# Kernel tuning notes

Hardware: AMD Instinct MI355X
Metric: run time of the kernel (lower is better)

Reference implementation:

```python
import jax, jax.numpy as jnp
import numpy as np

IDIM, NCH, ODIM = 512, 256, 3
B, W = 64, 1024


def _gru_cell(x, h, w_ih, w_hh, b_ih, b_hh):
    # PyTorch GRU gate order: r, z, n
    gi = x @ w_ih.T + b_ih
    gh = h @ w_hh.T + b_hh
    i_r, i_z, i_n = jnp.split(gi, 3, axis=-1)
    h_r, h_z, h_n = jnp.split(gh, 3, axis=-1)
    r = jax.nn.sigmoid(i_r + h_r)
    z = jax.nn.sigmoid(i_z + h_z)
    n = jnp.tanh(i_n + r * h_n)
    return (1.0 - z) * n + z * h


def setup_inputs() -> dict:
    key = jax.random.key(0)
    ks = jax.random.split(key, 14)
    s = 0.05
    return {
        "x": jax.random.normal(ks[0], (B, W, IDIM), dtype=jnp.float32),
        "embed_w": jax.random.normal(ks[1], (NCH, ODIM), dtype=jnp.float32) * s,
        "embed_b": jnp.zeros((NCH,), dtype=jnp.float32),
        "w_ih0": jax.random.normal(ks[2], (3 * NCH, IDIM + NCH), dtype=jnp.float32) * s,
        "w_hh0": jax.random.normal(ks[3], (3 * NCH, NCH), dtype=jnp.float32) * s,
        "b_ih0": jnp.zeros((3 * NCH,), dtype=jnp.float32),
        "b_hh0": jnp.zeros((3 * NCH,), dtype=jnp.float32),
        "w_ih1": jax.random.normal(ks[4], (3 * NCH, NCH), dtype=jnp.float32) * s,
        "w_hh1": jax.random.normal(ks[5], (3 * NCH, NCH), dtype=jnp.float32) * s,
        "b_ih1": jnp.zeros((3 * NCH,), dtype=jnp.float32),
        "b_hh1": jnp.zeros((3 * NCH,), dtype=jnp.float32),
        "proj_w": jax.random.normal(ks[6], (ODIM, NCH), dtype=jnp.float32) * s,
        "proj_b": jnp.zeros((ODIM,), dtype=jnp.float32),
    }


def reference(x, embed_w, embed_b, w_ih0, w_hh0, b_ih0, b_hh0,
              w_ih1, w_hh1, b_ih1, b_hh1, proj_w, proj_b):
    # at each step t, embed previous sigmoid VAD output, concat with x_t,
    # run 2-layer GRU single step, project + sigmoid.
    b = x.shape[0]
    h0_init = jnp.zeros((b, NCH), dtype=x.dtype)
    h1_init = jnp.zeros((b, NCH), dtype=x.dtype)
    v_init = jnp.zeros((b, ODIM), dtype=x.dtype)

    def step(carry, x_t):
        h0, h1, prev_v = carry
        emb = prev_v @ embed_w.T + embed_b                 # [B, NCH]
        inp = jnp.concatenate([x_t, emb], axis=-1)         # [B, IDIM+NCH]
        h0 = _gru_cell(inp, h0, w_ih0, w_hh0, b_ih0, b_hh0)
        h1 = _gru_cell(h0, h1, w_ih1, w_hh1, b_ih1, b_hh1)
        v = jax.nn.sigmoid(h1 @ proj_w.T + proj_b)         # [B, ODIM]
        return (h0, h1, v), v

    xs = jnp.transpose(x, (1, 0, 2))  # [W, B, IDIM]
    _, ys = jax.lax.scan(step, (h0_init, h1_init, v_init), xs)
    return jnp.transpose(ys, (1, 0, 2))  # [B, W, ODIM]
```

## Files before the change

kernel.cpp:

```cpp
#include <hip/hip_runtime.h>

#define T_FULL 1024
#define NBATCH 64
#define IDIM   512
#define NCH    256
#define GD     768
#define ODIM   3
#define NBLK   16

typedef _Float16 half8   __attribute__((ext_vector_type(8)));
typedef float    floatx4 __attribute__((ext_vector_type(4)));

__device__ __forceinline__ float sigmoidf_(float x) { return 1.0f / (1.0f + __expf(-x)); }
__device__ __forceinline__ float tanhf_(float x)    { return 1.0f - 2.0f / (__expf(2.0f * x) + 1.0f); }

__device__ __forceinline__ floatx4 splat4(float v) { floatx4 r; r[0]=v; r[1]=v; r[2]=v; r[3]=v; return r; }

__device__ __forceinline__ half8 cvt8(const float* __restrict__ p) {
  floatx4 a = *(const floatx4*)p;
  floatx4 b = *(const floatx4*)(p + 4);
  half8 h;
  h[0]=(_Float16)a[0]; h[1]=(_Float16)a[1]; h[2]=(_Float16)a[2]; h[3]=(_Float16)a[3];
  h[4]=(_Float16)b[0]; h[5]=(_Float16)b[1]; h[6]=(_Float16)b[2]; h[7]=(_Float16)b[3];
  return h;
}

__global__ __launch_bounds__(256)
void xw_gemm(const float* __restrict__ x, const float* __restrict__ w_ih0,
             _Float16* __restrict__ Xw, int t0, int Tc) {
  __shared__ _Float16 As[128 * 32];
  __shared__ _Float16 Bs[128 * 32];
  const int tid  = threadIdx.x;
  const int lane = tid & 63;
  const int wave = tid >> 6;
  const int lq = lane >> 4, lc = lane & 15;
  const int wm = wave >> 1, wn = wave & 1;

  const int sr = tid >> 1;
  const int sh = (tid & 1) * 16;
  const int m  = blockIdx.x * 128 + sr;
  const float* arow = x + ((size_t)(m & 63) * T_FULL + (size_t)(t0 + (m >> 6))) * IDIM;
  const float* brow = w_ih0 + (size_t)(blockIdx.y * 128 + sr) * GD;

  floatx4 acc[4][4];
  #pragma unroll
  for (int i = 0; i < 4; ++i)
    #pragma unroll
    for (int j = 0; j < 4; ++j) acc[i][j] = splat4(0.f);

  for (int kk = 0; kk < IDIM; kk += 32) {
    __syncthreads();
    #pragma unroll
    for (int kb = 0; kb < 2; ++kb) {
      const int k0  = sh + kb * 8;
      const int gis = (k0 >> 3) ^ ((sr >> 2) & 3);
      *(half8*)((char*)As + sr * 64 + gis * 16) = cvt8(arow + kk + k0);
      *(half8*)((char*)Bs + sr * 64 + gis * 16) = cvt8(brow + kk + k0);
    }
    __syncthreads();
    half8 af[4], bf[4];
    #pragma unroll
    for (int ms = 0; ms < 4; ++ms) {
      const int r = wm * 64 + ms * 16 + lc;
      af[ms] = *(const half8*)((char*)As + r * 64 + ((lq ^ ((r >> 2) & 3)) * 16));
    }
    #pragma unroll
    for (int ns = 0; ns < 4; ++ns) {
      const int r = wn * 64 + ns * 16 + lc;
      bf[ns] = *(const half8*)((char*)Bs + r * 64 + ((lq ^ ((r >> 2) & 3)) * 16));
    }
    #pragma unroll
    for (int ms = 0; ms < 4; ++ms)
      #pragma unroll
      for (int ns = 0; ns < 4; ++ns)
        acc[ms][ns] = __builtin_amdgcn_mfma_f32_16x16x32_f16(af[ms], bf[ns], acc[ms][ns], 0, 0, 0);
  }

  #pragma unroll
  for (int ms = 0; ms < 4; ++ms)
    #pragma unroll
    for (int ns = 0; ns < 4; ++ns)
      #pragma unroll
      for (int q = 0; q < 4; ++q) {
        const int mloc = blockIdx.x * 128 + wm * 64 + ms * 16 + lq * 4 + q;
        const int g    = blockIdx.y * 128 + wn * 64 + ns * 16 + lc;
        Xw[(size_t)mloc * GD + g] = (_Float16)acc[ms][ns][q];
      }
}

__device__ __forceinline__ void grid_barrier(unsigned int* flags, int blk, unsigned int ep) {
  __syncthreads();
  if (threadIdx.x == 0) {
    __builtin_amdgcn_fence(__ATOMIC_RELEASE, "agent");
    __hip_atomic_store(&flags[blk * 32], ep, __ATOMIC_RELAXED, __HIP_MEMORY_SCOPE_AGENT);
  }
  if (threadIdx.x < 64) {
    const int lane = threadIdx.x;
    const int idx  = (lane < NBLK) ? lane * 32 : 0;
    int spins = 0;
    for (;;) {
      unsigned int v = __hip_atomic_load(&flags[idx], __ATOMIC_RELAXED, __HIP_MEMORY_SCOPE_AGENT);
      if (lane >= NBLK) v = ep;
      if (__all((int)(v >= ep))) break;
      if (++spins > (1 << 16)) break;
      __builtin_amdgcn_s_sleep(1);
    }
    __builtin_amdgcn_fence(__ATOMIC_ACQUIRE, "agent");
  }
  __syncthreads();
}

__global__ __launch_bounds__(256, 1)
void rec_step(const float* __restrict__ w_ih0, const float* __restrict__ w_hh0,
              const float* __restrict__ w_ih1, const float* __restrict__ w_hh1,
              const float* __restrict__ b_ih0, const float* __restrict__ b_hh0,
              const float* __restrict__ b_ih1, const float* __restrict__ b_hh1,
              const float* __restrict__ embed_w, const float* __restrict__ embed_b,
              const float* __restrict__ proj_w, const float* __restrict__ proj_b,
              const _Float16* __restrict__ Xw, float* __restrict__ out,
              _Float16* h0_pub, _Float16* h1_pub, unsigned int* flags,
              int t0, int Tc, int lastChunk) {
  const int tid  = threadIdx.x;
  const int wave = tid >> 6;
  const int lane = tid & 63;
  const int lq = lane >> 4, lc = lane & 15;
  const int blk = blockIdx.x;
  const int c   = blk * 16 + lc;

  half8 Whh0[3][8], Whh1[3][8], Wih1[3][8], Pj[8];
  #pragma unroll
  for (int g = 0; g < 3; ++g) {
    const int row = g * NCH + c;
    #pragma unroll
    for (int ks = 0; ks < 8; ++ks) {
      const int k0 = ks * 32 + lq * 8;
      Whh0[g][ks] = cvt8(w_hh0 + (size_t)row * NCH + k0);
      Whh1[g][ks] = cvt8(w_hh1 + (size_t)row * NCH + k0);
      Wih1[g][ks] = cvt8(w_ih1 + (size_t)row * NCH + k0);
    }
  }
  #pragma unroll
  for (int ks = 0; ks < 8; ++ks) {
    const int k0 = ks * 32 + lq * 8;
    half8 z;
    #pragma unroll
    for (int j = 0; j < 8; ++j) z[j] = (_Float16)0.f;
    Pj[ks] = (lc < 3) ? cvt8(proj_w + lc * NCH + k0) : z;
  }

  float Wce[3][3], bi0[3], bh0v[3], bi1v[3], bh1v[3];
  #pragma unroll
  for (int g = 0; g < 3; ++g) {
    const int row = g * NCH + c;
    float a0 = 0.f, a1 = 0.f, a2 = 0.f, ab = b_ih0[row];
    const float* wr = w_ih0 + (size_t)row * GD + IDIM;
    for (int k = 0; k < NCH; ++k) {
      const float w = wr[k];
      a0 += w * embed_w[k * 3 + 0];
      a1 += w * embed_w[k * 3 + 1];
      a2 += w * embed_w[k * 3 + 2];
      ab += w * embed_b[k];
    }
    Wce[g][0] = a0; Wce[g][1] = a1; Wce[g][2] = a2;
    bi0[g] = ab;
    bh0v[g] = b_hh0[row]; bi1v[g] = b_ih1[row]; bh1v[g] = b_hh1[row];
  }
  const float pb = (lc < 3) ? proj_b[lc] : 0.f;

  float h0st[4] = {0.f, 0.f, 0.f, 0.f};
  float h1st[4] = {0.f, 0.f, 0.f, 0.f};
  if (t0 > 0) {
    const int rp0 = ((t0 & 1) ^ 1) * (NBATCH * NCH);
    #pragma unroll
    for (int q = 0; q < 4; ++q) {
      const int b = wave * 16 + lq * 4 + q;
      h0st[q] = (float)h0_pub[rp0 + b * NCH + c];
      h1st[q] = (float)h1_pub[rp0 + b * NCH + c];
    }
  }
  floatx4 ag1[3];
  const int arow = (wave * 16 + lc) * NCH;

  for (int lt = 0; lt < Tc; ++lt) {
    const int gt = t0 + lt;
    const int rp = ((gt & 1) ^ 1) * (NBATCH * NCH);
    const int wp = (gt & 1) * (NBATCH * NCH);
    const _Float16* h0r = h0_pub + rp;
    const _Float16* h1r = h1_pub + rp;

    floatx4 ah0[3];
    #pragma unroll
    for (int g = 0; g < 3; ++g) ah0[g] = splat4(bh0v[g]);
    #pragma unroll
    for (int hh = 0; hh < 2; ++hh) {
      half8 ha[4];
      #pragma unroll
      for (int i = 0; i < 4; ++i) ha[i] = *(const half8*)(h0r + arow + (hh * 4 + i) * 32 + lq * 8);
      #pragma unroll
      for (int g = 0; g < 3; ++g)
        #pragma unroll
        for (int i = 0; i < 4; ++i)
          ah0[g] = __builtin_amdgcn_mfma_f32_16x16x32_f16(ha[i], Whh0[g][hh * 4 + i], ah0[g], 0, 0, 0);
    }
    #pragma unroll
    for (int g = 0; g < 3; ++g) ag1[g] = splat4(bh1v[g]);
    floatx4 av = splat4(pb);
    #pragma unroll
    for (int hh = 0; hh < 2; ++hh) {
      half8 ha[4];
      #pragma unroll
      for (int i = 0; i < 4; ++i) ha[i] = *(const half8*)(h1r + arow + (hh * 4 + i) * 32 + lq * 8);
      #pragma unroll
      for (int g = 0; g < 3; ++g)
        #pragma unroll
        for (int i = 0; i < 4; ++i)
          ag1[g] = __builtin_amdgcn_mfma_f32_16x16x32_f16(ha[i], Whh1[g][hh * 4 + i], ag1[g], 0, 0, 0);
      #pragma unroll
      for (int i = 0; i < 4; ++i)
        av = __builtin_amdgcn_mfma_f32_16x16x32_f16(ha[i], Pj[hh * 4 + i], av, 0, 0, 0);
    }
    float vv0[4], vv1[4], vv2[4];
    if (gt == 0) {
      #pragma unroll
      for (int q = 0; q < 4; ++q) { vv0[q] = 0.f; vv1[q] = 0.f; vv2[q] = 0.f; }
    } else {
      float sv[4];
      #pragma unroll
      for (int q = 0; q < 4; ++q) sv[q] = (lc < 3) ? sigmoidf_(av[q]) : 0.f;
      if (blk == 0 && lc < 3) {
        #pragma unroll
        for (int q = 0; q < 4; ++q)
          out[((size_t)(wave * 16 + lq * 4 + q) * T_FULL + (gt - 1)) * ODIM + lc] = sv[q];
      }
      #pragma unroll
      for (int q = 0; q < 4; ++q) {
        vv0[q] = __shfl(sv[q], (lq << 4) + 0, 64);
        vv1[q] = __shfl(sv[q], (lq << 4) + 1, 64);
        vv2[q] = __shfl(sv[q], (lq << 4) + 2, 64);
      }
    }
    const _Float16* xwp = Xw + (size_t)lt * (NBATCH * GD);
    float h0n[4];
    #pragma unroll
    for (int q = 0; q < 4; ++q) {
      const int b = wave * 16 + lq * 4 + q;
      const float i_r = (float)xwp[b * GD + 0 * NCH + c] + bi0[0] + vv0[q] * Wce[0][0] + vv1[q] * Wce[0][1] + vv2[q] * Wce[0][2];
      const float i_z = (float)xwp[b * GD + 1 * NCH + c] + bi0[1] + vv0[q] * Wce[1][0] + vv1[q] * Wce[1][1] + vv2[q] * Wce[1][2];
      const float i_n = (float)xwp[b * GD + 2 * NCH + c] + bi0[2] + vv0[q] * Wce[2][0] + vv1[q] * Wce[2][1] + vv2[q] * Wce[2][2];
      const float r = sigmoidf_(i_r + ah0[0][q]);
      const float z = sigmoidf_(i_z + ah0[1][q]);
      const float n = tanhf_(i_n + r * ah0[2][q]);
      h0n[q] = (1.f - z) * n + z * h0st[q];
      h0st[q] = h0n[q];
    }
    {
      _Float16* h0w = h0_pub + wp;
      #pragma unroll
      for (int q = 0; q < 4; ++q)
        h0w[(wave * 16 + lq * 4 + q) * NCH + c] = (_Float16)h0n[q];
    }
    grid_barrier(flags, blk, (unsigned)(2 * gt + 1));

    const _Float16* h0r2 = h0_pub + wp;
    floatx4 ai1[3];
    #pragma unroll
    for (int g = 0; g < 3; ++g) ai1[g] = splat4(bi1v[g]);
    #pragma unroll
    for (int hh = 0; hh < 2; ++hh) {
      half8 ha[4];
      #pragma unroll
      for (int i = 0; i < 4; ++i) ha[i] = *(const half8*)(h0r2 + arow + (hh * 4 + i) * 32 + lq * 8);
      #pragma unroll
      for (int g = 0; g < 3; ++g)
        #pragma unroll
        for (int i = 0; i < 4; ++i)
          ai1[g] = __builtin_amdgcn_mfma_f32_16x16x32_f16(ha[i], Wih1[g][hh * 4 + i], ai1[g], 0, 0, 0);
    }
    float h1n[4];
    #pragma unroll
    for (int q = 0; q < 4; ++q) {
      const float r = sigmoidf_(ai1[0][q] + ag1[0][q]);
      const float z = sigmoidf_(ai1[1][q] + ag1[1][q]);
      const float n = tanhf_(ai1[2][q] + r * ag1[2][q]);
      h1n[q] = (1.f - z) * n + z * h1st[q];
      h1st[q] = h1n[q];
    }
    {
      _Float16* h1w = h1_pub + wp;
      #pragma unroll
      for (int q = 0; q < 4; ++q)
        h1w[(wave * 16 + lq * 4 + q) * NCH + c] = (_Float16)h1n[q];
    }
    grid_barrier(flags, blk, (unsigned)(2 * gt + 2));
  }

  if (lastChunk && blk == 0) {
    const _Float16* h1r = h1_pub + (((t0 + Tc - 1) & 1)) * (NBATCH * NCH);
    floatx4 av = splat4(pb);
    #pragma unroll
    for (int ks = 0; ks < 8; ++ks) {
      half8 ha = *(const half8*)(h1r + arow + ks * 32 + lq * 8);
      av = __builtin_amdgcn_mfma_f32_16x16x32_f16(ha, Pj[ks], av, 0, 0, 0);
    }
    if (lc < 3) {
      #pragma unroll
      for (int q = 0; q < 4; ++q)
        out[((size_t)(wave * 16 + lq * 4 + q) * T_FULL + (T_FULL - 1)) * ODIM + lc] = sigmoidf_(av[q]);
    }
  }
}

extern "C" void kernel_launch(void* const* d_in, const int* in_sizes, int n_in,
                              void* d_out, int out_size, void* d_ws, size_t ws_size,
                              hipStream_t stream) {
  const float* x       = (const float*)d_in[0];
  const float* embed_w = (const float*)d_in[1];
  const float* embed_b = (const float*)d_in[2];
  const float* w_ih0   = (const float*)d_in[3];
  const float* w_hh0   = (const float*)d_in[4];
  const float* b_ih0   = (const float*)d_in[5];
  const float* b_hh0   = (const float*)d_in[6];
  const float* w_ih1   = (const float*)d_in[7];
  const float* w_hh1   = (const float*)d_in[8];
  const float* b_ih1   = (const float*)d_in[9];
  const float* b_hh1   = (const float*)d_in[10];
  const float* proj_w  = (const float*)d_in[11];
  const float* proj_b  = (const float*)d_in[12];
  float* out = (float*)d_out;

  char* ws = (char*)d_ws;
  _Float16* h0_pub = (_Float16*)(ws);
  _Float16* h1_pub = (_Float16*)(ws + 65536);
  unsigned int* flags = (unsigned int*)(ws + 131072);
  _Float16* Xw = (_Float16*)(ws + 262144);

  const size_t per_t = (size_t)NBATCH * GD * sizeof(_Float16);
  size_t xw_avail = (ws_size > 262144) ? (ws_size - 262144) : 0;
  long maxTc = (long)(xw_avail / per_t);
  int Tc = 2;
  while ((long)Tc * 2 <= maxTc && Tc * 2 <= T_FULL) Tc *= 2;

  hipMemsetAsync(ws, 0, 262144, stream);

  for (int t0 = 0; t0 < T_FULL; t0 += Tc) {
    dim3 g1(Tc * NBATCH / 128, GD / 128);
    xw_gemm<<<g1, 256, 0, stream>>>(x, w_ih0, Xw, t0, Tc);
    rec_step<<<NBLK, 256, 0, stream>>>(w_ih0, w_hh0, w_ih1, w_hh1,
                                       b_ih0, b_hh0, b_ih1, b_hh1,
                                       embed_w, embed_b, proj_w, proj_b,
                                       Xw, out, h0_pub, h1_pub, flags,
                                       t0, Tc, (t0 + Tc) >= T_FULL ? 1 : 0);
  }
}
```

Before: 10.19 ms.

## Replace grid barriers with tagged hidden-state publish and per-wave polling

Removes the flag-based grid barrier. Each hidden-state value is now published as a 64-bit word holding the fp16 data pair plus a timestep tag. Consumers poll directly on the data with cache-bypassing loads until all tags match, so sync and data transfer are fused and each wave waits only for what it needs. The Xw layout is rearranged so each block reads a contiguous per-block tile, and the h1 work is reordered ahead of h0. This doubles the bytes moved for state and adds spin-polling traffic, and the bounded spin can silently read stale data on timeout.

```diff
diff --git a/kernel.cpp b/kernel.cpp
--- a/kernel.cpp
+++ b/kernel.cpp
@@ -10,10 +10,11 @@
 
 typedef _Float16 half8   __attribute__((ext_vector_type(8)));
 typedef float    floatx4 __attribute__((ext_vector_type(4)));
+typedef unsigned int uintx4 __attribute__((ext_vector_type(4)));
+typedef unsigned int uintx2 __attribute__((ext_vector_type(2)));
 
 __device__ __forceinline__ float sigmoidf_(float x) { return 1.0f / (1.0f + __expf(-x)); }
 __device__ __forceinline__ float tanhf_(float x)    { return 1.0f - 2.0f / (__expf(2.0f * x) + 1.0f); }
-
 __device__ __forceinline__ floatx4 splat4(float v) { floatx4 r; r[0]=v; r[1]=v; r[2]=v; r[3]=v; return r; }
 
 __device__ __forceinline__ half8 cvt8(const float* __restrict__ p) {
@@ -83,31 +84,65 @@
       #pragma unroll
       for (int q = 0; q < 4; ++q) {
         const int mloc = blockIdx.x * 128 + wm * 64 + ms * 16 + lq * 4 + q;
-        const int g    = blockIdx.y * 128 + wn * 64 + ns * 16 + lc;
-        Xw[(size_t)mloc * GD + g] = (_Float16)acc[ms][ns][q];
+        const int gp   = blockIdx.y * 128 + wn * 64 + ns * 16 + lc;
+        const int t = mloc >> 6, b = mloc & 63;
+        const int gate = gp >> 8, cch = gp & 255;
+        Xw[(((size_t)t * NBLK + (cch >> 4)) * 3 + gate) * 1024 + b * 16 + (cch & 15)]
+            = (_Float16)acc[ms][ns][q];
       }
 }
 
-__device__ __forceinline__ void grid_barrier(unsigned int* flags, int blk, unsigned int ep) {
-  __syncthreads();
-  if (threadIdx.x == 0) {
-    __builtin_amdgcn_fence(__ATOMIC_RELEASE, "agent");
-    __hip_atomic_store(&flags[blk * 32], ep, __ATOMIC_RELAXED, __HIP_MEMORY_SCOPE_AGENT);
-  }
-  if (threadIdx.x < 64) {
-    const int lane = threadIdx.x;
-    const int idx  = (lane < NBLK) ? lane * 32 : 0;
-    int spins = 0;
-    for (;;) {
-      unsigned int v = __hip_atomic_load(&flags[idx], __ATOMIC_RELAXED, __HIP_MEMORY_SCOPE_AGENT);
-      if (lane >= NBLK) v = ep;
-      if (__all((int)(v >= ep))) break;
-      if (++spins > (1 << 16)) break;
-      __builtin_amdgcn_s_sleep(1);
-    }
-    __builtin_amdgcn_fence(__ATOMIC_ACQUIRE, "agent");
-  }
-  __syncthreads();
+__device__ __forceinline__ void poll_group(const char* __restrict__ pb, int boff,
+                                           unsigned exp, half8* __restrict__ out) {
+  uintx4 A[16];
+  int cap = 1 << 18;
+  for (;;) {
+    #pragma unroll
+    for (int f = 0; f < 8; ++f) {
+      const char* p0 = pb + boff + f * 128;
+      asm volatile("global_load_dwordx4 %0, %1, off sc0 sc1"
+                   : "=v"(A[2 * f]) : "v"(p0) : "memory");
+      asm volatile("global_load_dwordx4 %0, %1, off sc0 sc1"
+                   : "=v"(A[2 * f + 1]) : "v"(p0 + 16) : "memory");
+    }
+    asm volatile("s_waitcnt vmcnt(0)" ::: "memory");
+    __builtin_amdgcn_sched_barrier(0);
+    bool ok = true;
+    #pragma unroll
+    for (int j = 0; j < 16; ++j) ok = ok && (A[j].y == exp) && (A[j].w == exp);
+    if (__all((int)ok) || --cap <= 0) break;
+  }
+  #pragma unroll
+  for (int f = 0; f < 8; ++f) {
+    uintx4 t;
+    t.x = A[2 * f].x;     t.y = A[2 * f].z;
+    t.z = A[2 * f + 1].x; t.w = A[2 * f + 1].z;
+    out[f] = __builtin_bit_cast(half8, t);
+  }
+}
+
+__device__ __forceinline__ void publish4(char* __restrict__ base, int wave, int lq, int lc,
+                                         int blk, unsigned tag, const float* __restrict__ hv) {
+  float pv[4];
+  #pragma unroll
+  for (int q = 0; q < 4; ++q) pv[q] = __shfl_xor(hv[q], 1, 64);
+  unsigned dq[4];
+  #pragma unroll
+  for (int q = 0; q < 4; ++q) {
+    _Float16 a = (_Float16)hv[q], p = (_Float16)pv[q];
+    unsigned au = __builtin_bit_cast(unsigned short, a);
+    unsigned pu = __builtin_bit_cast(unsigned short, p);
+    dq[q] = (lc & 1) ? (pu | (au << 16)) : (au | (pu << 16));
+  }
+  const int q0 = (lc & 1) ? 2 : 0;
+  #pragma unroll
+  for (int s = 0; s < 2; ++s) {
+    const int q = q0 + s;
+    char* addr = base + (((wave * 16 + lq * 4 + q) * 128) + blk * 8 + (lc >> 1)) * 8;
+    uintx2 v; v.x = dq[q]; v.y = tag;
+    asm volatile("global_store_dwordx2 %0, %1, off sc0 sc1"
+                 :: "v"(addr), "v"(v) : "memory");
+  }
 }
 
 __global__ __launch_bounds__(256, 1)
@@ -118,7 +153,7 @@
               const float* __restrict__ embed_w, const float* __restrict__ embed_b,
               const float* __restrict__ proj_w, const float* __restrict__ proj_b,
               const _Float16* __restrict__ Xw, float* __restrict__ out,
-              _Float16* h0_pub, _Float16* h1_pub, unsigned int* flags,
+              char* h0b, char* h1b,
               int t0, int Tc, int lastChunk) {
   const int tid  = threadIdx.x;
   const int wave = tid >> 6;
@@ -170,55 +205,61 @@
   float h0st[4] = {0.f, 0.f, 0.f, 0.f};
   float h1st[4] = {0.f, 0.f, 0.f, 0.f};
   if (t0 > 0) {
-    const int rp0 = ((t0 & 1) ^ 1) * (NBATCH * NCH);
+    const int rpo = ((t0 & 1) ^ 1) * 65536;
+    const unsigned long long* p0 = (const unsigned long long*)(h0b + rpo);
+    const unsigned long long* p1 = (const unsigned long long*)(h1b + rpo);
     #pragma unroll
     for (int q = 0; q < 4; ++q) {
-      const int b = wave * 16 + lq * 4 + q;
-      h0st[q] = (float)h0_pub[rp0 + b * NCH + c];
-      h1st[q] = (float)h1_pub[rp0 + b * NCH + c];
-    }
-  }
-  floatx4 ag1[3];
-  const int arow = (wave * 16 + lc) * NCH;
+      const int b   = wave * 16 + lq * 4 + q;
+      const int idx = b * 128 + blk * 8 + (lc >> 1);
+      unsigned d0 = (unsigned)p0[idx], d1 = (unsigned)p1[idx];
+      unsigned short u0 = (lc & 1) ? (unsigned short)(d0 >> 16) : (unsigned short)(d0 & 0xffff);
+      unsigned short u1 = (lc & 1) ? (unsigned short)(d1 >> 16) : (unsigned short)(d1 & 0xffff);
+      h0st[q] = (float)__builtin_bit_cast(_Float16, u0);
+      h1st[q] = (float)__builtin_bit_cast(_Float16, u1);
+    }
+  }
+
+  const int boff = (wave * 16 + lc) * 1024 + lq * 32;
+  floatx4 ag1l[3];
+  half8 hf[8];
 
   for (int lt = 0; lt < Tc; ++lt) {
     const int gt = t0 + lt;
-    const int rp = ((gt & 1) ^ 1) * (NBATCH * NCH);
-    const int wp = (gt & 1) * (NBATCH * NCH);
-    const _Float16* h0r = h0_pub + rp;
-    const _Float16* h1r = h1_pub + rp;
-
+    const int rp = ((gt & 1) ^ 1) * 65536;
+    const int wp = (gt & 1) * 65536;
+    const unsigned expt = (unsigned)gt;
+
+    const _Float16* xb = Xw + ((size_t)lt * NBLK + blk) * 3072;
+    unsigned short xwu[3][4];
+    #pragma unroll
+    for (int g = 0; g < 3; ++g)
+      #pragma unroll
+      for (int q = 0; q < 4; ++q)
+        xwu[g][q] = *(const unsigned short*)(xb + g * 1024 + (wave * 16 + lq * 4 + q) * 16 + lc);
+
+    poll_group(h1b + rp, boff, expt, hf);
+    floatx4 av = splat4(pb);
+    #pragma unroll
+    for (int g = 0; g < 3; ++g) ag1l[g] = splat4(bh1v[g]);
+    #pragma unroll
+    for (int ks = 0; ks < 8; ++ks) {
+      #pragma unroll
+      for (int g = 0; g < 3; ++g)
+        ag1l[g] = __builtin_amdgcn_mfma_f32_16x16x32_f16(hf[ks], Whh1[g][ks], ag1l[g], 0, 0, 0);
+      av = __builtin_amdgcn_mfma_f32_16x16x32_f16(hf[ks], Pj[ks], av, 0, 0, 0);
+    }
+
+    poll_group(h0b + rp, boff, expt, hf);
     floatx4 ah0[3];
     #pragma unroll
     for (int g = 0; g < 3; ++g) ah0[g] = splat4(bh0v[g]);
     #pragma unroll
-    for (int hh = 0; hh < 2; ++hh) {
-      half8 ha[4];
-      #pragma unroll
-      for (int i = 0; i < 4; ++i) ha[i] = *(const half8*)(h0r + arow + (hh * 4 + i) * 32 + lq * 8);
+    for (int ks = 0; ks < 8; ++ks)
       #pragma unroll
       for (int g = 0; g < 3; ++g)
-        #pragma unroll
-        for (int i = 0; i < 4; ++i)
-          ah0[g] = __builtin_amdgcn_mfma_f32_16x16x32_f16(ha[i], Whh0[g][hh * 4 + i], ah0[g], 0, 0, 0);
-    }
-    #pragma unroll
-    for (int g = 0; g < 3; ++g) ag1[g] = splat4(bh1v[g]);
-    floatx4 av = splat4(pb);
-    #pragma unroll
-    for (int hh = 0; hh < 2; ++hh) {
-      half8 ha[4];
-      #pragma unroll
-      for (int i = 0; i < 4; ++i) ha[i] = *(const half8*)(h1r + arow + (hh * 4 + i) * 32 + lq * 8);
-      #pragma unroll
-      for (int g = 0; g < 3; ++g)
-        #pragma unroll
-        for (int i = 0; i < 4; ++i)
-          ag1[g] = __builtin_amdgcn_mfma_f32_16x16x32_f16(ha[i], Whh1[g][hh * 4 + i], ag1[g], 0, 0, 0);
-      #pragma unroll
-      for (int i = 0; i < 4; ++i)
-        av = __builtin_amdgcn_mfma_f32_16x16x32_f16(ha[i], Pj[hh * 4 + i], av, 0, 0, 0);
-    }
+        ah0[g] = __builtin_amdgcn_mfma_f32_16x16x32_f16(hf[ks], Whh0[g][ks], ah0[g], 0, 0, 0);
+
     float vv0[4], vv1[4], vv2[4];
     if (gt == 0) {
       #pragma unroll
@@ -239,73 +280,57 @@
         vv2[q] = __shfl(sv[q], (lq << 4) + 2, 64);
       }
     }
-    const _Float16* xwp = Xw + (size_t)lt * (NBATCH * GD);
+
     float h0n[4];
     #pragma unroll
     for (int q = 0; q < 4; ++q) {
-      const int b = wave * 16 + lq * 4 + q;
-      const float i_r = (float)xwp[b * GD + 0 * NCH + c] + bi0[0] + vv0[q] * Wce[0][0] + vv1[q] * Wce[0][1] + vv2[q] * Wce[0][2];
-      const float i_z = (float)xwp[b * GD + 1 * NCH + c] + bi0[1] + vv0[q] * Wce[1][0] + vv1[q] * Wce[1][1] + vv2[q] * Wce[1][2];
-      const float i_n = (float)xwp[b * GD + 2 * NCH + c] + bi0[2] + vv0[q] * Wce[2][0] + vv1[q] * Wce[2][1] + vv2[q] * Wce[2][2];
+      const float i_r = (float)__builtin_bit_cast(_Float16, xwu[0][q]) + bi0[0]
+                        + vv0[q] * Wce[0][0] + vv1[q] * Wce[0][1] + vv2[q] * Wce[0][2];
+      const float i_z = (float)__builtin_bit_cast(_Float16, xwu[1][q]) + bi0[1]
+                        + vv0[q] * Wce[1][0] + vv1[q] * Wce[1][1] + vv2[q] * Wce[1][2];
+      const float i_n = (float)__builtin_bit_cast(_Float16, xwu[2][q]) + bi0[2]
+                        + vv0[q] * Wce[2][0] + vv1[q] * Wce[2][1] + vv2[q] * Wce[2][2];
       const float r = sigmoidf_(i_r + ah0[0][q]);
       const float z = sigmoidf_(i_z + ah0[1][q]);
       const float n = tanhf_(i_n + r * ah0[2][q]);
       h0n[q] = (1.f - z) * n + z * h0st[q];
       h0st[q] = h0n[q];
     }
-    {
-      _Float16* h0w = h0_pub + wp;
-      #pragma unroll
-      for (int q = 0; q < 4; ++q)
-        h0w[(wave * 16 + lq * 4 + q) * NCH + c] = (_Float16)h0n[q];
-    }
-    grid_barrier(flags, blk, (unsigned)(2 * gt + 1));
-
-    const _Float16* h0r2 = h0_pub + wp;
+    publish4(h0b + wp, wave, lq, lc, blk, (unsigned)(gt + 1), h0n);
+
+    poll_group(h0b + wp, boff, (unsigned)(gt + 1), hf);
     floatx4 ai1[3];
     #pragma unroll
     for (int g = 0; g < 3; ++g) ai1[g] = splat4(bi1v[g]);
     #pragma unroll
-    for (int hh = 0; hh < 2; ++hh) {
-      half8 ha[4];
-      #pragma unroll
-      for (int i = 0; i < 4; ++i) ha[i] = *(const half8*)(h0r2 + arow + (hh * 4 + i) * 32 + lq * 8);
+    for (int ks = 0; ks < 8; ++ks)
       #pragma unroll
       for (int g = 0; g < 3; ++g)
-        #pragma unroll
-        for (int i = 0; i < 4; ++i)
-          ai1[g] = __builtin_amdgcn_mfma_f32_16x16x32_f16(ha[i], Wih1[g][hh * 4 + i], ai1[g], 0, 0, 0);
-    }
+        ai1[g] = __builtin_amdgcn_mfma_f32_16x16x32_f16(hf[ks], Wih1[g][ks], ai1[g], 0, 0, 0);
+
     float h1n[4];
     #pragma unroll
     for (int q = 0; q < 4; ++q) {
-      const float r = sigmoidf_(ai1[0][q] + ag1[0][q]);
-      const float z = sigmoidf_(ai1[1][q] + ag1[1][q]);
-      const float n = tanhf_(ai1[2][q] + r * ag1[2][q]);
+      const float r = sigmoidf_(ai1[0][q] + ag1l[0][q]);
+      const float z = sigmoidf_(ai1[1][q] + ag1l[1][q]);
+      const float n = tanhf_(ai1[2][q] + r * ag1l[2][q]);
       h1n[q] = (1.f - z) * n + z * h1st[q];
       h1st[q] = h1n[q];
     }
-    {
-      _Float16* h1w = h1_pub + wp;
+    publish4(h1b + wp, wave, lq, lc, blk, (unsigned)(gt + 1), h1n);
+  }
+
+  if (lastChunk && blk == 0) {
+    poll_group(h1b + (((t0 + Tc - 1) & 1) * 65536), boff, (unsigned)(t0 + Tc), hf);
+    floatx4 av = splat4(pb);
+    #pragma unroll
+    for (int ks = 0; ks < 8; ++ks)
+      av = __builtin_amdgcn_mfma_f32_16x16x32_f16(hf[ks], Pj[ks], av, 0, 0, 0);
+    if (lc < 3) {
       #pragma unroll
       for (int q = 0; q < 4; ++q)
-        h1w[(wave * 16 + lq * 4 + q) * NCH + c] = (_Float16)h1n[q];
-    }
-    grid_barrier(flags, blk, (unsigned)(2 * gt + 2));
-  }
-
-  if (lastChunk && blk == 0) {
-    const _Float16* h1r = h1_pub + (((t0 + Tc - 1) & 1)) * (NBATCH * NCH);
-    floatx4 av = splat4(pb);
-    #pragma unroll
-    for (int ks = 0; ks < 8; ++ks) {
-      half8 ha = *(const half8*)(h1r + arow + ks * 32 + lq * 8);
-      av = __builtin_amdgcn_mfma_f32_16x16x32_f16(ha, Pj[ks], av, 0, 0, 0);
-    }
-    if (lc < 3) {
-      #pragma unroll
-      for (int q = 0; q < 4; ++q)
-        out[((size_t)(wave * 16 + lq * 4 + q) * T_FULL + (T_FULL - 1)) * ODIM + lc] = sigmoidf_(av[q]);
+        out[((size_t)(wave * 16 + lq * 4 + q) * T_FULL + (T_FULL - 1)) * ODIM + lc]
+            = sigmoidf_(av[q]);
     }
   }
 }
@@ -329,9 +354,8 @@
   float* out = (float*)d_out;
 
   char* ws = (char*)d_ws;
-  _Float16* h0_pub = (_Float16*)(ws);
-  _Float16* h1_pub = (_Float16*)(ws + 65536);
-  unsigned int* flags = (unsigned int*)(ws + 131072);
+  char* h0b = ws;
+  char* h1b = ws + 131072;
   _Float16* Xw = (_Float16*)(ws + 262144);
 
   const size_t per_t = (size_t)NBATCH * GD * sizeof(_Float16);
@@ -348,7 +372,7 @@
     rec_step<<<NBLK, 256, 0, stream>>>(w_ih0, w_hh0, w_ih1, w_hh1,
                                        b_ih0, b_hh0, b_ih1, b_hh1,
                                        embed_w, embed_b, proj_w, proj_b,
-                                       Xw, out, h0_pub, h1_pub, flags,
+                                       Xw, out, h0b, h1b,
                                        t0, Tc, (t0 + Tc) >= T_FULL ? 1 : 0);
   }
 }
```

New measurement: 14.12 ms. +38.6%, slower.

## Split recurrence by batch groups with LDS-resident hidden state, drop grid barriers

Applied to the files above, without the earlier changes.

The recurrent kernel is reorganized so each of 4 workgroups (1024 threads) owns 16 batch rows and all 256 channels. Hidden state is exchanged through double-buffered swizzled LDS, and workgroup __syncthreads replace the cross-block atomic grid barriers. Weight conversion to fp16 in MFMA fragment order and the embedding fold are moved into separate prep kernels. The input-projection GEMM now writes in a tiled layout matching the new fragments. The aim is to remove the global-memory flag spins every timestep, but each workgroup now holds all weights in registers with only 4 CUs active, and large register arrays per thread risk spills.

```diff
diff --git a/kernel.cpp b/kernel.cpp
--- a/kernel.cpp
+++ b/kernel.cpp
@@ -6,14 +6,19 @@
 #define NCH    256
 #define GD     768
 #define ODIM   3
-#define NBLK   16
-
-typedef _Float16 half8   __attribute__((ext_vector_type(8)));
+#define NBG    4
+
+typedef _Float16 half8 __attribute__((ext_vector_type(8)));
+typedef _Float16 half4 __attribute__((ext_vector_type(4)));
 typedef float    floatx4 __attribute__((ext_vector_type(4)));
+
+#define PP_OFF   1179648
+#define WCB_OFF  1187840
+#define HS_OFF   1200128
+#define XW_OFF   1376256
 
 __device__ __forceinline__ float sigmoidf_(float x) { return 1.0f / (1.0f + __expf(-x)); }
 __device__ __forceinline__ float tanhf_(float x)    { return 1.0f - 2.0f / (__expf(2.0f * x) + 1.0f); }
-
 __device__ __forceinline__ floatx4 splat4(float v) { floatx4 r; r[0]=v; r[1]=v; r[2]=v; r[3]=v; return r; }
 
 __device__ __forceinline__ half8 cvt8(const float* __restrict__ p) {
@@ -23,6 +28,53 @@
   h[0]=(_Float16)a[0]; h[1]=(_Float16)a[1]; h[2]=(_Float16)a[2]; h[3]=(_Float16)a[3];
   h[4]=(_Float16)b[0]; h[5]=(_Float16)b[1]; h[6]=(_Float16)b[2]; h[7]=(_Float16)b[3];
   return h;
+}
+
+__global__ __launch_bounds__(256)
+void wprep_w(const float* __restrict__ w_hh0, const float* __restrict__ w_ih1,
+             const float* __restrict__ w_hh1, const float* __restrict__ proj_w,
+             _Float16* __restrict__ Wp, _Float16* __restrict__ Pp) {
+  const int idx = blockIdx.x * 256 + threadIdx.x;
+  if (idx < 73728) {
+    const int m = idx / 24576, r = idx % 24576;
+    const int pt = r / 512, r2 = r % 512;
+    const int ks = r2 / 64, lane = r2 % 64;
+    const int lq = lane >> 4, lc = lane & 15;
+    const int c = (pt / 3) * 16 + lc, g = pt % 3;
+    const float* src = (m == 0 ? w_hh0 : (m == 1 ? w_ih1 : w_hh1))
+                       + (size_t)(g * NCH + c) * NCH + ks * 32 + lq * 8;
+    *(half8*)(Wp + (size_t)idx * 8) = cvt8(src);
+  } else if (idx < 74240) {
+    const int j = idx - 73728;
+    const int ks = j >> 6, lane = j & 63;
+    const int lq = lane >> 4, lc = lane & 15;
+    half8 v;
+    if (lc < 3) v = cvt8(proj_w + lc * NCH + ks * 32 + lq * 8);
+    else { for (int k = 0; k < 8; ++k) v[k] = (_Float16)0.f; }
+    *(half8*)(Pp + (size_t)j * 8) = v;
+  }
+}
+
+__global__ __launch_bounds__(256)
+void wprep_c(const float* __restrict__ w_ih0, const float* __restrict__ embed_w,
+             const float* __restrict__ embed_b, const float* __restrict__ b_ih0,
+             float* __restrict__ Wcb) {
+  const int prow = blockIdx.x * 256 + threadIdx.x;
+  if (prow >= 768) return;
+  const int pt = prow >> 4, lcc = prow & 15;
+  const int c = (pt / 3) * 16 + lcc, g = pt % 3;
+  const int srow = g * NCH + c;
+  const float* wr = w_ih0 + (size_t)srow * GD + IDIM;
+  float a0 = 0.f, a1 = 0.f, a2 = 0.f, ab = b_ih0[srow];
+  for (int k = 0; k < NCH; ++k) {
+    const float w = wr[k];
+    a0 += w * embed_w[k * 3 + 0];
+    a1 += w * embed_w[k * 3 + 1];
+    a2 += w * embed_w[k * 3 + 2];
+    ab += w * embed_b[k];
+  }
+  Wcb[prow * 4 + 0] = a0; Wcb[prow * 4 + 1] = a1;
+  Wcb[prow * 4 + 2] = a2; Wcb[prow * 4 + 3] = ab;
 }
 
 __global__ __launch_bounds__(256)
@@ -83,231 +135,195 @@
       #pragma unroll
       for (int q = 0; q < 4; ++q) {
         const int mloc = blockIdx.x * 128 + wm * 64 + ms * 16 + lq * 4 + q;
-        const int g    = blockIdx.y * 128 + wn * 64 + ns * 16 + lc;
-        Xw[(size_t)mloc * GD + g] = (_Float16)acc[ms][ns][q];
+        const int gp   = blockIdx.y * 128 + wn * 64 + ns * 16 + lc;
+        const int t = mloc >> 6, b = mloc & 63;
+        const int g = gp >> 8, c = gp & 255;
+        const int pt = (c >> 4) * 3 + g;
+        Xw[(((size_t)t * NBG + (b >> 4)) * 48 + pt) * 256 + (c & 15) * 16 + (b & 15)]
+            = (_Float16)acc[ms][ns][q];
       }
 }
 
-__device__ __forceinline__ void grid_barrier(unsigned int* flags, int blk, unsigned int ep) {
-  __syncthreads();
-  if (threadIdx.x == 0) {
-    __builtin_amdgcn_fence(__ATOMIC_RELEASE, "agent");
-    __hip_atomic_store(&flags[blk * 32], ep, __ATOMIC_RELAXED, __HIP_MEMORY_SCOPE_AGENT);
-  }
-  if (threadIdx.x < 64) {
-    const int lane = threadIdx.x;
-    const int idx  = (lane < NBLK) ? lane * 32 : 0;
-    int spins = 0;
-    for (;;) {
-      unsigned int v = __hip_atomic_load(&flags[idx], __ATOMIC_RELAXED, __HIP_MEMORY_SCOPE_AGENT);
-      if (lane >= NBLK) v = ep;
-      if (__all((int)(v >= ep))) break;
-      if (++spins > (1 << 16)) break;
-      __builtin_amdgcn_s_sleep(1);
-    }
-    __builtin_amdgcn_fence(__ATOMIC_ACQUIRE, "agent");
-  }
-  __syncthreads();
-}
-
-__global__ __launch_bounds__(256, 1)
-void rec_step(const float* __restrict__ w_ih0, const float* __restrict__ w_hh0,
-              const float* __restrict__ w_ih1, const float* __restrict__ w_hh1,
-              const float* __restrict__ b_ih0, const float* __restrict__ b_hh0,
-              const float* __restrict__ b_ih1, const float* __restrict__ b_hh1,
-              const float* __restrict__ embed_w, const float* __restrict__ embed_b,
-              const float* __restrict__ proj_w, const float* __restrict__ proj_b,
-              const _Float16* __restrict__ Xw, float* __restrict__ out,
-              _Float16* h0_pub, _Float16* h1_pub, unsigned int* flags,
-              int t0, int Tc, int lastChunk) {
+__global__ __launch_bounds__(1024, 4)
+void rec_r(const _Float16* __restrict__ Wp, const _Float16* __restrict__ Pp,
+           const float* __restrict__ Wcb,
+           const float* __restrict__ b_hh0, const float* __restrict__ b_ih1,
+           const float* __restrict__ b_hh1, const float* __restrict__ proj_b,
+           const _Float16* __restrict__ Xw, float* __restrict__ out,
+           float* __restrict__ hs, int t0, int Tc, int lastChunk) {
+  __shared__ __align__(16) _Float16 hl[2][2][4096];
+  __shared__ __align__(16) float v_lds[64];
   const int tid  = threadIdx.x;
   const int wave = tid >> 6;
   const int lane = tid & 63;
   const int lq = lane >> 4, lc = lane & 15;
-  const int blk = blockIdx.x;
-  const int c   = blk * 16 + lc;
-
-  half8 Whh0[3][8], Whh1[3][8], Wih1[3][8], Pj[8];
+  const int bg = blockIdx.x;
+  const int ch = wave * 16 + lc;
+
+  #define HBYTE(b, k) ((b) * 512 + (((k) * 2) ^ (((b) & 7) << 4)))
+  #define LDA(layer, par, ks) \
+    (*(const half8*)((const char*)(&hl[layer][par][0]) + lc * 512 + ((((ks) * 64) + lq * 16) ^ ((lc & 7) << 4))))
+
+  half8 W0[3][8], W1[3][8], W2[3][8], Pj[8];
+  #pragma unroll
+  for (int g = 0; g < 3; ++g)
+    #pragma unroll
+    for (int ks = 0; ks < 8; ++ks) {
+      const size_t base = ((size_t)(wave * 3 + g) * 512 + ks * 64 + lane) * 8;
+      W0[g][ks] = *(const half8*)(Wp + base);
+      W1[g][ks] = *(const half8*)(Wp + 196608 + base);
+      W2[g][ks] = *(const half8*)(Wp + 393216 + base);
+    }
+  #pragma unroll
+  for (int ks = 0; ks < 8; ++ks)
+    Pj[ks] = *(const half8*)(Pp + ((size_t)ks * 64 + lane) * 8);
+
+  float wcb[3][4], bh0c[3], bi1c[3], bh1c[3];
   #pragma unroll
   for (int g = 0; g < 3; ++g) {
-    const int row = g * NCH + c;
-    #pragma unroll
-    for (int ks = 0; ks < 8; ++ks) {
-      const int k0 = ks * 32 + lq * 8;
-      Whh0[g][ks] = cvt8(w_hh0 + (size_t)row * NCH + k0);
-      Whh1[g][ks] = cvt8(w_hh1 + (size_t)row * NCH + k0);
-      Wih1[g][ks] = cvt8(w_ih1 + (size_t)row * NCH + k0);
-    }
-  }
-  #pragma unroll
-  for (int ks = 0; ks < 8; ++ks) {
-    const int k0 = ks * 32 + lq * 8;
-    half8 z;
-    #pragma unroll
-    for (int j = 0; j < 8; ++j) z[j] = (_Float16)0.f;
-    Pj[ks] = (lc < 3) ? cvt8(proj_w + lc * NCH + k0) : z;
-  }
-
-  float Wce[3][3], bi0[3], bh0v[3], bi1v[3], bh1v[3];
-  #pragma unroll
-  for (int g = 0; g < 3; ++g) {
-    const int row = g * NCH + c;
-    float a0 = 0.f, a1 = 0.f, a2 = 0.f, ab = b_ih0[row];
-    const float* wr = w_ih0 + (size_t)row * GD + IDIM;
-    for (int k = 0; k < NCH; ++k) {
-      const float w = wr[k];
-      a0 += w * embed_w[k * 3 + 0];
-      a1 += w * embed_w[k * 3 + 1];
-      a2 += w * embed_w[k * 3 + 2];
-      ab += w * embed_b[k];
-    }
-    Wce[g][0] = a0; Wce[g][1] = a1; Wce[g][2] = a2;
-    bi0[g] = ab;
-    bh0v[g] = b_hh0[row]; bi1v[g] = b_ih1[row]; bh1v[g] = b_hh1[row];
+    floatx4 t = *(const floatx4*)(Wcb + ((size_t)((wave * 3 + g) * 16 + lc)) * 4);
+    wcb[g][0] = t[0]; wcb[g][1] = t[1]; wcb[g][2] = t[2]; wcb[g][3] = t[3];
+    const int srow = g * NCH + ch;
+    bh0c[g] = b_hh0[srow]; bi1c[g] = b_ih1[srow]; bh1c[g] = b_hh1[srow];
   }
   const float pb = (lc < 3) ? proj_b[lc] : 0.f;
 
-  float h0st[4] = {0.f, 0.f, 0.f, 0.f};
-  float h1st[4] = {0.f, 0.f, 0.f, 0.f};
+  float h0st[4] = {0.f,0.f,0.f,0.f};
+  float h1st[4] = {0.f,0.f,0.f,0.f};
   if (t0 > 0) {
-    const int rp0 = ((t0 & 1) ^ 1) * (NBATCH * NCH);
     #pragma unroll
     for (int q = 0; q < 4; ++q) {
-      const int b = wave * 16 + lq * 4 + q;
-      h0st[q] = (float)h0_pub[rp0 + b * NCH + c];
-      h1st[q] = (float)h1_pub[rp0 + b * NCH + c];
-    }
-  }
-  floatx4 ag1[3];
-  const int arow = (wave * 16 + lc) * NCH;
+      h0st[q] = hs[((size_t)(bg * 2 + 0) * 16 + lq * 4 + q) * NCH + ch];
+      h1st[q] = hs[((size_t)(bg * 2 + 1) * 16 + lq * 4 + q) * NCH + ch];
+    }
+  }
+  const int pInit = (t0 & 1) ^ 1;
+  #pragma unroll
+  for (int q = 0; q < 4; ++q) {
+    const int b = lq * 4 + q;
+    *(_Float16*)((char*)(&hl[0][pInit][0]) + HBYTE(b, ch)) = (_Float16)h0st[q];
+    *(_Float16*)((char*)(&hl[1][pInit][0]) + HBYTE(b, ch)) = (_Float16)h1st[q];
+  }
+  __syncthreads();
 
   for (int lt = 0; lt < Tc; ++lt) {
     const int gt = t0 + lt;
-    const int rp = ((gt & 1) ^ 1) * (NBATCH * NCH);
-    const int wp = (gt & 1) * (NBATCH * NCH);
-    const _Float16* h0r = h0_pub + rp;
-    const _Float16* h1r = h1_pub + rp;
-
-    floatx4 ah0[3];
-    #pragma unroll
-    for (int g = 0; g < 3; ++g) ah0[g] = splat4(bh0v[g]);
-    #pragma unroll
-    for (int hh = 0; hh < 2; ++hh) {
-      half8 ha[4];
-      #pragma unroll
-      for (int i = 0; i < 4; ++i) ha[i] = *(const half8*)(h0r + arow + (hh * 4 + i) * 32 + lq * 8);
-      #pragma unroll
-      for (int g = 0; g < 3; ++g)
-        #pragma unroll
-        for (int i = 0; i < 4; ++i)
-          ah0[g] = __builtin_amdgcn_mfma_f32_16x16x32_f16(ha[i], Whh0[g][hh * 4 + i], ah0[g], 0, 0, 0);
-    }
-    #pragma unroll
-    for (int g = 0; g < 3; ++g) ag1[g] = splat4(bh1v[g]);
+    const int rp = (gt & 1) ^ 1;
+    const int wp = gt & 1;
+
+    const _Float16* xb = Xw + ((((size_t)lt * NBG + bg) * 48 + wave * 3) * 256)
+                         + lc * 16 + lq * 4;
+    half4 xwv[3];
+    #pragma unroll
+    for (int g = 0; g < 3; ++g) xwv[g] = *(const half4*)(xb + g * 256);
+
+    half8 A1f[8], A0f[8];
+    #pragma unroll
+    for (int ks = 0; ks < 8; ++ks) { A1f[ks] = LDA(1, rp, ks); A0f[ks] = LDA(0, rp, ks); }
+
+    if (wave == 0 && gt > 0) {
+      floatx4 av = splat4(pb);
+      #pragma unroll
+      for (int ks = 0; ks < 8; ++ks)
+        av = __builtin_amdgcn_mfma_f32_16x16x32_f16(A1f[ks], Pj[ks], av, 0, 0, 0);
+      #pragma unroll
+      for (int q = 0; q < 4; ++q) {
+        if (lc < 3) {
+          const float sv = sigmoidf_(av[q]);
+          v_lds[(lq * 4 + q) * 4 + lc] = sv;
+          out[((size_t)(bg * 16 + lq * 4 + q) * T_FULL + (gt - 1)) * ODIM + lc] = sv;
+        }
+      }
+    }
+
+    floatx4 ag1[3], ag0[3];
+    #pragma unroll
+    for (int g = 0; g < 3; ++g) { ag1[g] = splat4(bh1c[g]); ag0[g] = splat4(bh0c[g]); }
+    #pragma unroll
+    for (int g = 0; g < 3; ++g)
+      #pragma unroll
+      for (int ks = 0; ks < 8; ++ks)
+        ag1[g] = __builtin_amdgcn_mfma_f32_16x16x32_f16(A1f[ks], W2[g][ks], ag1[g], 0, 0, 0);
+    #pragma unroll
+    for (int g = 0; g < 3; ++g)
+      #pragma unroll
+      for (int ks = 0; ks < 8; ++ks)
+        ag0[g] = __builtin_amdgcn_mfma_f32_16x16x32_f16(A0f[ks], W0[g][ks], ag0[g], 0, 0, 0);
+
+    __syncthreads();
+
+    floatx4 v4[4];
+    if (gt == 0) {
+      #pragma unroll
+      for (int q = 0; q < 4; ++q) v4[q] = splat4(0.f);
+    } else {
+      #pragma unroll
+      for (int q = 0; q < 4; ++q) v4[q] = *(const floatx4*)(&v_lds[(lq * 4 + q) * 4]);
+    }
+
+    #pragma unroll
+    for (int q = 0; q < 4; ++q) {
+      const float ir = (float)xwv[0][q] + wcb[0][3]
+                       + v4[q][0] * wcb[0][0] + v4[q][1] * wcb[0][1] + v4[q][2] * wcb[0][2];
+      const float iz = (float)xwv[1][q] + wcb[1][3]
+                       + v4[q][0] * wcb[1][0] + v4[q][1] * wcb[1][1] + v4[q][2] * wcb[1][2];
+      const float in_ = (float)xwv[2][q] + wcb[2][3]
+                       + v4[q][0] * wcb[2][0] + v4[q][1] * wcb[2][1] + v4[q][2] * wcb[2][2];
+      const float r = sigmoidf_(ir + ag0[0][q]);
+      const float z = sigmoidf_(iz + ag0[1][q]);
+      const float n = tanhf_(in_ + r * ag0[2][q]);
+      const float h0n = (1.f - z) * n + z * h0st[q];
+      h0st[q] = h0n;
+      *(_Float16*)((char*)(&hl[0][wp][0]) + HBYTE(lq * 4 + q, ch)) = (_Float16)h0n;
+    }
+    __syncthreads();
+
+    half8 A0n[8];
+    #pragma unroll
+    for (int ks = 0; ks < 8; ++ks) A0n[ks] = LDA(0, wp, ks);
+
+    floatx4 ai[3];
+    #pragma unroll
+    for (int g = 0; g < 3; ++g) ai[g] = splat4(bi1c[g]);
+    #pragma unroll
+    for (int g = 0; g < 3; ++g)
+      #pragma unroll
+      for (int ks = 0; ks < 8; ++ks)
+        ai[g] = __builtin_amdgcn_mfma_f32_16x16x32_f16(A0n[ks], W1[g][ks], ai[g], 0, 0, 0);
+
+    #pragma unroll
+    for (int q = 0; q < 4; ++q) {
+      const float r = sigmoidf_(ai[0][q] + ag1[0][q]);
+      const float z = sigmoidf_(ai[1][q] + ag1[1][q]);
+      const float n = tanhf_(ai[2][q] + r * ag1[2][q]);
+      const float h1n = (1.f - z) * n + z * h1st[q];
+      h1st[q] = h1n;
+      *(_Float16*)((char*)(&hl[1][wp][0]) + HBYTE(lq * 4 + q, ch)) = (_Float16)h1n;
+    }
+    __syncthreads();
+  }
+
+  if (lastChunk && wave == 0) {
+    const int fp = (t0 + Tc - 1) & 1;
     floatx4 av = splat4(pb);
     #pragma unroll
-    for (int hh = 0; hh < 2; ++hh) {
-      half8 ha[4];
-      #pragma unroll
-      for (int i = 0; i < 4; ++i) ha[i] = *(const half8*)(h1r + arow + (hh * 4 + i) * 32 + lq * 8);
-      #pragma unroll
-      for (int g = 0; g < 3; ++g)
-        #pragma unroll
-        for (int i = 0; i < 4; ++i)
-          ag1[g] = __builtin_amdgcn_mfma_f32_16x16x32_f16(ha[i], Whh1[g][hh * 4 + i], ag1[g], 0, 0, 0);
-      #pragma unroll
-      for (int i = 0; i < 4; ++i)
-        av = __builtin_amdgcn_mfma_f32_16x16x32_f16(ha[i], Pj[hh * 4 + i], av, 0, 0, 0);
-    }
-    float vv0[4], vv1[4], vv2[4];
-    if (gt == 0) {
-      #pragma unroll
-      for (int q = 0; q < 4; ++q) { vv0[q] = 0.f; vv1[q] = 0.f; vv2[q] = 0.f; }
-    } else {
-      float sv[4];
-      #pragma unroll
-      for (int q = 0; q < 4; ++q) sv[q] = (lc < 3) ? sigmoidf_(av[q]) : 0.f;
-      if (blk == 0 && lc < 3) {
-        #pragma unroll
-        for (int q = 0; q < 4; ++q)
-          out[((size_t)(wave * 16 + lq * 4 + q) * T_FULL + (gt - 1)) * ODIM + lc] = sv[q];
-      }
-      #pragma unroll
-      for (int q = 0; q < 4; ++q) {
-        vv0[q] = __shfl(sv[q], (lq << 4) + 0, 64);
-        vv1[q] = __shfl(sv[q], (lq << 4) + 1, 64);
-        vv2[q] = __shfl(sv[q], (lq << 4) + 2, 64);
-      }
-    }
-    const _Float16* xwp = Xw + (size_t)lt * (NBATCH * GD);
-    float h0n[4];
-    #pragma unroll
-    for (int q = 0; q < 4; ++q) {
-      const int b = wave * 16 + lq * 4 + q;
-      const float i_r = (float)xwp[b * GD + 0 * NCH + c] + bi0[0] + vv0[q] * Wce[0][0] + vv1[q] * Wce[0][1] + vv2[q] * Wce[0][2];
-      const float i_z = (float)xwp[b * GD + 1 * NCH + c] + bi0[1] + vv0[q] * Wce[1][0] + vv1[q] * Wce[1][1] + vv2[q] * Wce[1][2];
-      const float i_n = (float)xwp[b * GD + 2 * NCH + c] + bi0[2] + vv0[q] * Wce[2][0] + vv1[q] * Wce[2][1] + vv2[q] * Wce[2][2];
-      const float r = sigmoidf_(i_r + ah0[0][q]);
-      const float z = sigmoidf_(i_z + ah0[1][q]);
-      const float n = tanhf_(i_n + r * ah0[2][q]);
-      h0n[q] = (1.f - z) * n + z * h0st[q];
-      h0st[q] = h0n[q];
-    }
-    {
-      _Float16* h0w = h0_pub + wp;
+    for (int ks = 0; ks < 8; ++ks)
+      av = __builtin_amdgcn_mfma_f32_16x16x32_f16(LDA(1, fp, ks), Pj[ks], av, 0, 0, 0);
+    if (lc < 3) {
       #pragma unroll
       for (int q = 0; q < 4; ++q)
-        h0w[(wave * 16 + lq * 4 + q) * NCH + c] = (_Float16)h0n[q];
-    }
-    grid_barrier(flags, blk, (unsigned)(2 * gt + 1));
-
-    const _Float16* h0r2 = h0_pub + wp;
-    floatx4 ai1[3];
-    #pragma unroll
-    for (int g = 0; g < 3; ++g) ai1[g] = splat4(bi1v[g]);
-    #pragma unroll
-    for (int hh = 0; hh < 2; ++hh) {
-      half8 ha[4];
-      #pragma unroll
-      for (int i = 0; i < 4; ++i) ha[i] = *(const half8*)(h0r2 + arow + (hh * 4 + i) * 32 + lq * 8);
-      #pragma unroll
-      for (int g = 0; g < 3; ++g)
-        #pragma unroll
-        for (int i = 0; i < 4; ++i)
-          ai1[g] = __builtin_amdgcn_mfma_f32_16x16x32_f16(ha[i], Wih1[g][hh * 4 + i], ai1[g], 0, 0, 0);
-    }
-    float h1n[4];
-    #pragma unroll
-    for (int q = 0; q < 4; ++q) {
-      const float r = sigmoidf_(ai1[0][q] + ag1[0][q]);
-      const float z = sigmoidf_(ai1[1][q] + ag1[1][q]);
-      const float n = tanhf_(ai1[2][q] + r * ag1[2][q]);
-      h1n[q] = (1.f - z) * n + z * h1st[q];
-      h1st[q] = h1n[q];
-    }
-    {
-      _Float16* h1w = h1_pub + wp;
-      #pragma unroll
-      for (int q = 0; q < 4; ++q)
-        h1w[(wave * 16 + lq * 4 + q) * NCH + c] = (_Float16)h1n[q];
-    }
-    grid_barrier(flags, blk, (unsigned)(2 * gt + 2));
-  }
-
-  if (lastChunk && blk == 0) {
-    const _Float16* h1r = h1_pub + (((t0 + Tc - 1) & 1)) * (NBATCH * NCH);
-    floatx4 av = splat4(pb);
-    #pragma unroll
-    for (int ks = 0; ks < 8; ++ks) {
-      half8 ha = *(const half8*)(h1r + arow + ks * 32 + lq * 8);
-      av = __builtin_amdgcn_mfma_f32_16x16x32_f16(ha, Pj[ks], av, 0, 0, 0);
-    }
-    if (lc < 3) {
-      #pragma unroll
-      for (int q = 0; q < 4; ++q)
-        out[((size_t)(wave * 16 + lq * 4 + q) * T_FULL + (T_FULL - 1)) * ODIM + lc] = sigmoidf_(av[q]);
-    }
-  }
+        out[((size_t)(bg * 16 + lq * 4 + q) * T_FULL + (T_FULL - 1)) * ODIM + lc]
+            = sigmoidf_(av[q]);
+    }
+  }
+
+  #pragma unroll
+  for (int q = 0; q < 4; ++q) {
+    hs[((size_t)(bg * 2 + 0) * 16 + lq * 4 + q) * NCH + ch] = h0st[q];
+    hs[((size_t)(bg * 2 + 1) * 16 + lq * 4 + q) * NCH + ch] = h1st[q];
+  }
+  #undef HBYTE
+  #undef LDA
 }
 
 extern "C" void kernel_launch(void* const* d_in, const int* in_sizes, int n_in,
@@ -329,26 +345,26 @@
   float* out = (float*)d_out;
 
   char* ws = (char*)d_ws;
-  _Float16* h0_pub = (_Float16*)(ws);
-  _Float16* h1_pub = (_Float16*)(ws + 65536);
-  unsigned int* flags = (unsigned int*)(ws + 131072);
-  _Float16* Xw = (_Float16*)(ws + 262144);
+  _Float16* Wp  = (_Float16*)ws;
+  _Float16* Pp  = (_Float16*)(ws + PP_OFF);
+  float*    Wcb = (float*)(ws + WCB_OFF);
+  float*    hs  = (float*)(ws + HS_OFF);
+  _Float16* Xw  = (_Float16*)(ws + XW_OFF);
+
+  wprep_w<<<290, 256, 0, stream>>>(w_hh0, w_ih1, w_hh1, proj_w, Wp, Pp);
+  wprep_c<<<3, 256, 0, stream>>>(w_ih0, embed_w, embed_b, b_ih0, Wcb);
 
   const size_t per_t = (size_t)NBATCH * GD * sizeof(_Float16);
-  size_t xw_avail = (ws_size > 262144) ? (ws_size - 262144) : 0;
+  size_t xw_avail = (ws_size > XW_OFF) ? (ws_size - XW_OFF) : 0;
   long maxTc = (long)(xw_avail / per_t);
   int Tc = 2;
   while ((long)Tc * 2 <= maxTc && Tc * 2 <= T_FULL) Tc *= 2;
 
-  hipMemsetAsync(ws, 0, 262144, stream);
-
   for (int t0 = 0; t0 < T_FULL; t0 += Tc) {
     dim3 g1(Tc * NBATCH / 128, GD / 128);
     xw_gemm<<<g1, 256, 0, stream>>>(x, w_ih0, Xw, t0, Tc);
-    rec_step<<<NBLK, 256, 0, stream>>>(w_ih0, w_hh0, w_ih1, w_hh1,
-                                       b_ih0, b_hh0, b_ih1, b_hh1,
-                                       embed_w, embed_b, proj_w, proj_b,
-                                       Xw, out, h0_pub, h1_pub, flags,
-                                       t0, Tc, (t0 + Tc) >= T_FULL ? 1 : 0);
-  }
-}
+    rec_r<<<NBG, 1024, 0, stream>>>(Wp, Pp, Wcb, b_hh0, b_ih1, b_hh1, proj_b,
+                                    Xw, out, hs, t0, Tc,
+                                    (t0 + Tc) >= T_FULL ? 1 : 0);
+  }
+}
```

Result: slower. 40.55 ms (+298.0%).
